# Performance work log

Measured on AMD Instinct MI355X. Metric: run time of the kernel, lower is better.

The kernel has to match this reference:

```python
import jax, jax.numpy as jnp
import numpy as np

N_NODES = 100000
N_EDGES = 800000
N_PAIRS = 500000
IN_DIM = 128
HID_DIM = 128
OUT_DIM = 64


def setup_inputs() -> dict:
    key = jax.random.key(0)
    k = jax.random.split(key, 7)
    x = jax.random.normal(k[0], (N_NODES, IN_DIM), dtype=jnp.float32)
    edge_rows = jax.random.randint(k[1], (N_EDGES,), 0, N_NODES, dtype=jnp.int32)
    edge_cols = jax.random.randint(k[2], (N_EDGES,), 0, N_NODES, dtype=jnp.int32)
    edge_vals = jax.random.uniform(k[3], (N_EDGES,), dtype=jnp.float32)
    pairs = jax.random.randint(k[4], (N_PAIRS, 2), 0, N_NODES, dtype=jnp.int32)
    # Learned params: nn.Linear(in, out, bias=False) -> weight applied as x @ W.T; we store W already transposed.
    W1 = jax.random.normal(k[5], (IN_DIM, HID_DIM), dtype=jnp.float32) / np.sqrt(IN_DIM)
    W2 = jax.random.normal(k[6], (HID_DIM, OUT_DIM), dtype=jnp.float32) / np.sqrt(HID_DIM)
    return {"x": x, "edge_rows": edge_rows, "edge_cols": edge_cols,
            "edge_vals": edge_vals, "pairs": pairs, "W1": W1, "W2": W2}


def reference(x, edge_rows, edge_cols, edge_vals, pairs, W1, W2):
    n = x.shape[0]

    def gcn(h, W):
        # SpMM: out[i] = sum_{e: rows[e]==i} vals[e] * h[cols[e]], then dense linear.
        msgs = edge_vals[:, None] * h[edge_cols]          # [E, d] gather
        agg = jax.ops.segment_sum(msgs, edge_rows, num_segments=n)  # [N, d] scatter
        return agg @ W

    h = jax.nn.relu(gcn(x, W1))
    h = gcn(h, W2)
    # decode: dot product between endpoint embeddings
    return jnp.sum(h[pairs[:, 0]] * h[pairs[:, 1]], axis=-1)  # [P]
```

## Files before the change

### kernel.cpp

```cpp
#include <hip/hip_runtime.h>

#define N_NODES 100000
#define N_EDGES 800000
#define N_PAIRS 500000

#define T_TILE  2048
#define N_TILES ((N_EDGES + T_TILE - 1) / T_TILE)
#define N_BKT   256
#define NPB     391
#define BCAP    4096

typedef _Float16 half4v __attribute__((ext_vector_type(4)));
typedef _Float16 half8v __attribute__((ext_vector_type(8)));
typedef float    f32x4  __attribute__((ext_vector_type(4)));

__device__ __forceinline__ int swz(int byte_off, int row) {
    return byte_off ^ ((row & 7) << 4);
}

template<int M, bool A_IS_F32>
__global__ __launch_bounds__(256) void gemm_mfma(const void* __restrict__ Ap,
                                                 const _Float16* __restrict__ Wt,
                                                 _Float16* __restrict__ C, int nRows) {
    constexpr int K  = 128;
    constexpr int CT = M / 16;
    __shared__ _Float16 Alds[64 * K];
    __shared__ _Float16 Wlds[M * K];

    const int rb = blockIdx.x * 64;

    if (A_IS_F32) {
        const float* A = (const float*)Ap;
        for (int idx = threadIdx.x; idx < 64 * (K / 4); idx += 256) {
            const int row = idx >> 5, c4 = idx & 31;
            const int rg = (rb + row < nRows) ? rb + row : nRows - 1;
            const float4 a = *(const float4*)&A[(long)rg * K + c4 * 4];
            half4v h = { (_Float16)a.x, (_Float16)a.y, (_Float16)a.z, (_Float16)a.w };
            *(half4v*)((char*)Alds + swz(row * 256 + c4 * 8, row)) = h;
        }
    } else {
        const _Float16* A = (const _Float16*)Ap;
        for (int idx = threadIdx.x; idx < 64 * (K / 8); idx += 256) {
            const int row = idx >> 4, seg = idx & 15;
            const int rg = (rb + row < nRows) ? rb + row : nRows - 1;
            const half8v h = *(const half8v*)&A[(long)rg * K + seg * 8];
            *(half8v*)((char*)Alds + swz(row * 256 + seg * 16, row)) = h;
        }
    }
    for (int idx = threadIdx.x; idx < M * (K / 8); idx += 256) {
        const int col = idx >> 4, seg = idx & 15;
        const half8v h = *(const half8v*)&Wt[col * K + seg * 8];
        *(half8v*)((char*)Wlds + swz(col * 256 + seg * 16, col)) = h;
    }
    __syncthreads();

    const int l  = threadIdx.x & 63;
    const int w  = threadIdx.x >> 6;
    const int lr = l & 15;
    const int lg = l >> 4;

    f32x4 acc[CT];
    #pragma unroll
    for (int ct = 0; ct < CT; ++ct) acc[ct] = (f32x4){0.f, 0.f, 0.f, 0.f};

    #pragma unroll
    for (int ks = 0; ks < K / 16; ++ks) {
        const int kb   = ks * 32 + lg * 8;
        const int arow = w * 16 + lr;
        const half4v af = *(const half4v*)((const char*)Alds + swz(arow * 256 + kb, arow));
        #pragma unroll
        for (int ct = 0; ct < CT; ++ct) {
            const int col = ct * 16 + lr;
            const half4v bf = *(const half4v*)((const char*)Wlds + swz(col * 256 + kb, col));
            acc[ct] = __builtin_amdgcn_mfma_f32_16x16x16f16(af, bf, acc[ct], 0, 0, 0);
        }
    }

    #pragma unroll
    for (int ct = 0; ct < CT; ++ct) {
        const int col = ct * 16 + lr;
        #pragma unroll
        for (int j = 0; j < 4; ++j) {
            const int row = rb + w * 16 + lg * 4 + j;
            if (row < nRows) C[(long)row * M + col] = (_Float16)acc[ct][j];
        }
    }
}

__global__ __launch_bounds__(512) void spmm_gemm_fused(const int* __restrict__ rowptr,
                                                       const long long* __restrict__ epack,
                                                       const _Float16* __restrict__ g,
                                                       const _Float16* __restrict__ Wt2,
                                                       _Float16* __restrict__ g2, int nRows) {
    constexpr int K = 128, M = 64;
    __shared__ _Float16 Alds[64 * K];
    __shared__ _Float16 Wlds[M * K];

    const int rb = blockIdx.x * 64;

    for (int idx = threadIdx.x; idx < M * (K / 8); idx += 512) {
        const int col = idx >> 4, seg = idx & 15;
        const half8v h = *(const half8v*)&Wt2[col * K + seg * 8];
        *(half8v*)((char*)Wlds + swz(col * 256 + seg * 16, col)) = h;
    }

    const int li = threadIdx.x & 15;
    const int rs = threadIdx.x >> 4;
    #pragma unroll
    for (int s = 0; s < 2; ++s) {
        const int lrow = s * 32 + rs;
        const int r  = rb + lrow;
        const int rc = (r < nRows) ? r : nRows - 1;
        const int lo = rowptr[rc], hi = rowptr[rc + 1];
        float acc[8] = {0.f, 0.f, 0.f, 0.f, 0.f, 0.f, 0.f, 0.f};
        #pragma unroll 4
        for (int e = lo; e < hi; ++e) {
            const long long pk = epack[e];
            const int   c = (int)pk;
            const float v = __int_as_float((int)(pk >> 32));
            const half8v m = *(const half8v*)&g[(long)c * K + li * 8];
            #pragma unroll
            for (int j = 0; j < 8; ++j) acc[j] += v * (float)m[j];
        }
        half8v h;
        #pragma unroll
        for (int j = 0; j < 8; ++j) h[j] = (_Float16)fmaxf(acc[j], 0.f);
        *(half8v*)((char*)Alds + swz(lrow * 256 + li * 16, lrow)) = h;
    }
    __syncthreads();

    const int l    = threadIdx.x & 63;
    const int w    = threadIdx.x >> 6;
    const int lr   = l & 15;
    const int lg   = l >> 4;
    const int rowg = w >> 1;
    const int colb = (w & 1) * 32;

    f32x4 acc[2];
    acc[0] = (f32x4){0.f, 0.f, 0.f, 0.f};
    acc[1] = (f32x4){0.f, 0.f, 0.f, 0.f};

    #pragma unroll
    for (int ks = 0; ks < K / 16; ++ks) {
        const int kb   = ks * 32 + lg * 8;
        const int arow = rowg * 16 + lr;
        const half4v af = *(const half4v*)((const char*)Alds + swz(arow * 256 + kb, arow));
        #pragma unroll
        for (int ct = 0; ct < 2; ++ct) {
            const int col = colb + ct * 16 + lr;
            const half4v bf = *(const half4v*)((const char*)Wlds + swz(col * 256 + kb, col));
            acc[ct] = __builtin_amdgcn_mfma_f32_16x16x16f16(af, bf, acc[ct], 0, 0, 0);
        }
    }

    #pragma unroll
    for (int ct = 0; ct < 2; ++ct) {
        const int col = colb + ct * 16 + lr;
        #pragma unroll
        for (int j = 0; j < 4; ++j) {
            const int row = rb + rowg * 16 + lg * 4 + j;
            if (row < nRows) g2[(long)row * M + col] = (_Float16)acc[ct][j];
        }
    }
}

__global__ __launch_bounds__(256) void hist_both(const int* __restrict__ erows,
                                                 int* __restrict__ hist,
                                                 const float* __restrict__ W1,
                                                 const float* __restrict__ W2,
                                                 _Float16* __restrict__ Wt1,
                                                 _Float16* __restrict__ Wt2) {
    if (blockIdx.x == N_TILES) {
        for (int i = threadIdx.x; i < 128 * 128; i += 256) {
            const int k = i >> 7, m = i & 127;
            Wt1[m * 128 + k] = (_Float16)W1[i];
        }
        for (int i = threadIdx.x; i < 128 * 64; i += 256) {
            const int k = i >> 6, m = i & 63;
            Wt2[m * 128 + k] = (_Float16)W2[i];
        }
        return;
    }
    __shared__ int cnt[N_BKT];
    cnt[threadIdx.x] = 0;
    __syncthreads();
    const int e0 = blockIdx.x * T_TILE;
    const int e1 = min(e0 + T_TILE, N_EDGES);
    for (int e = e0 + threadIdx.x; e < e1; e += 256)
        atomicAdd(&cnt[erows[e] / NPB], 1);
    __syncthreads();
    hist[blockIdx.x * N_BKT + threadIdx.x] = cnt[threadIdx.x];
}

__global__ __launch_bounds__(512) void bucket_scan(const int* __restrict__ hist,
                                                   int* __restrict__ offpart,
                                                   int* __restrict__ bt) {
    __shared__ int lds[512];
    const int b = blockIdx.x;
    const int t = threadIdx.x;
    const int v = (t < N_TILES) ? hist[t * N_BKT + b] : 0;
    lds[t] = v;
    __syncthreads();
    for (int o = 1; o < 512; o <<= 1) {
        int u = (t >= o) ? lds[t - o] : 0;
        __syncthreads();
        lds[t] += u;
        __syncthreads();
    }
    if (t < N_TILES) offpart[b * N_TILES + t] = lds[t] - v;
    if (t == 511) bt[b] = lds[511];
}

__global__ __launch_bounds__(256) void bkt_base(const int* __restrict__ bt,
                                                int* __restrict__ bbase) {
    __shared__ int lds[256];
    const int t = threadIdx.x;
    const int v = bt[t];
    lds[t] = v;
    __syncthreads();
    for (int o = 1; o < 256; o <<= 1) {
        int u = (t >= o) ? lds[t - o] : 0;
        __syncthreads();
        lds[t] += u;
        __syncthreads();
    }
    bbase[t] = lds[t] - v;
    if (t == 255) bbase[256] = lds[255];
}

__global__ __launch_bounds__(256) void partition(const int* __restrict__ erows,
                                                 const int* __restrict__ ecols,
                                                 const float* __restrict__ evals,
                                                 const int* __restrict__ offpart,
                                                 const int* __restrict__ bbase,
                                                 unsigned long long* __restrict__ etmp) {
    __shared__ int cur[N_BKT];
    cur[threadIdx.x] = bbase[threadIdx.x] + offpart[threadIdx.x * N_TILES + blockIdx.x];
    __syncthreads();
    const int e0 = blockIdx.x * T_TILE;
    const int e1 = min(e0 + T_TILE, N_EDGES);
    for (int e = e0 + threadIdx.x; e < e1; e += 256) {
        const int r = erows[e];
        const int b = r / NPB;
        const int lrow = r - b * NPB;
        const int p = atomicAdd(&cur[b], 1);
        etmp[p] = ((unsigned long long)(unsigned)__float_as_int(evals[e]) << 32)
                | ((unsigned)lrow << 17) | (unsigned)ecols[e];
    }
}

__global__ __launch_bounds__(256) void bucket_reorder(const int* __restrict__ bbase,
                                                      const unsigned long long* __restrict__ etmp,
                                                      unsigned long long* __restrict__ epack,
                                                      int* __restrict__ rowptr) {
    __shared__ int lcnt[NPB + 1];
    __shared__ int psum[256];
    __shared__ int lcur[NPB];
    __shared__ unsigned long long stg[BCAP];
    const int b    = blockIdx.x;
    const int t    = threadIdx.x;
    const int lo   = b * NPB;
    const int hiN  = min(lo + NPB, N_NODES);
    const int nloc = hiN - lo;
    const int base = bbase[b];
    const int cnt  = bbase[b + 1] - base;

    for (int j = t; j < NPB; j += 256) lcnt[j] = 0;
    __syncthreads();
    for (int i = t; i < cnt; i += 256)
        atomicAdd(&lcnt[(int)((etmp[base + i] >> 17) & 0x1FF)], 1);
    __syncthreads();
    const int j0 = 2 * t, j1 = 2 * t + 1;
    const int a0 = (j0 < NPB) ? lcnt[j0] : 0;
    const int a1 = (j1 < NPB) ? lcnt[j1] : 0;
    psum[t] = a0 + a1;
    __syncthreads();
    for (int o = 1; o < 256; o <<= 1) {
        int u = (t >= o) ? psum[t - o] : 0;
        __syncthreads();
        psum[t] += u;
        __syncthreads();
    }
    const int ex0 = psum[t] - (a0 + a1);
    const int ex1 = ex0 + a0;
    if (j0 < NPB) lcur[j0] = ex0;
    if (j1 < NPB) lcur[j1] = ex1;
    if (j0 < nloc) rowptr[lo + j0] = base + ex0;
    if (j1 < nloc) rowptr[lo + j1] = base + ex1;
    if (b == N_BKT - 1 && t == 0) rowptr[N_NODES] = N_EDGES;
    __syncthreads();
    for (int i = t; i < cnt; i += 256) {
        const unsigned long long p = etmp[base + i];
        const int lrow = (int)((p >> 17) & 0x1FF);
        const int pos  = atomicAdd(&lcur[lrow], 1);
        const unsigned long long rec = (p & 0xFFFFFFFF00000000ULL) | (p & 0x1FFFFULL);
        if (pos < BCAP) stg[pos] = rec;
        else epack[base + pos] = rec;
    }
    __syncthreads();
    const int n = min(cnt, BCAP);
    for (int i = t; i < n; i += 256)
        epack[base + i] = stg[i];
}

template<int D, bool RELU>
__global__ __launch_bounds__(256) void spmm_csr_h(const int* __restrict__ rowptr,
                                                  const long long* __restrict__ epack,
                                                  const _Float16* __restrict__ g,
                                                  _Float16* __restrict__ agg, int nRows) {
    constexpr int LPR = D / 8;
    constexpr int RPB = 256 / LPR;
    const int r  = blockIdx.x * RPB + threadIdx.x / LPR;
    const int li = threadIdx.x % LPR;
    if (r >= nRows) return;
    const int lo = rowptr[r], hi = rowptr[r + 1];
    float acc[8] = {0.f, 0.f, 0.f, 0.f, 0.f, 0.f, 0.f, 0.f};
    #pragma unroll 4
    for (int e = lo; e < hi; ++e) {
        const long long pk = epack[e];
        const int   c = (int)pk;
        const float v = __int_as_float((int)(pk >> 32));
        const half8v m = *(const half8v*)&g[(long)c * D + li * 8];
        #pragma unroll
        for (int j = 0; j < 8; ++j) acc[j] += v * (float)m[j];
    }
    half8v o;
    #pragma unroll
    for (int j = 0; j < 8; ++j) {
        float a = RELU ? fmaxf(acc[j], 0.f) : acc[j];
        o[j] = (_Float16)a;
    }
    *(half8v*)&agg[(long)r * D + li * 8] = o;
}

__global__ __launch_bounds__(256) void decode_dot(const _Float16* __restrict__ h2,
                                                  const int2* __restrict__ pairs,
                                                  float* __restrict__ out, int nPairs) {
    const int tid  = blockIdx.x * 256 + threadIdx.x;
    const int half = (nPairs + 1) / 2;
    const int p0   = tid >> 3;
    const int lane = tid & 7;
    if (p0 >= half) return;
    const int p1 = p0 + half;
    const bool has1 = p1 < nPairs;
    const int2 pr0 = pairs[p0];
    const int2 pr1 = has1 ? pairs[p1] : pr0;
    const half8v a0 = *(const half8v*)&h2[(long)pr0.x * 64 + lane * 8];
    const half8v b0 = *(const half8v*)&h2[(long)pr0.y * 64 + lane * 8];
    const half8v a1 = *(const half8v*)&h2[(long)pr1.x * 64 + lane * 8];
    const half8v b1 = *(const half8v*)&h2[(long)pr1.y * 64 + lane * 8];
    float s0 = 0.f, s1 = 0.f;
    #pragma unroll
    for (int j = 0; j < 8; ++j) {
        s0 += (float)a0[j] * (float)b0[j];
        s1 += (float)a1[j] * (float)b1[j];
    }
    s0 += __shfl_xor(s0, 1); s1 += __shfl_xor(s1, 1);
    s0 += __shfl_xor(s0, 2); s1 += __shfl_xor(s1, 2);
    s0 += __shfl_xor(s0, 4); s1 += __shfl_xor(s1, 4);
    if (lane == 0) {
        out[p0] = s0;
        if (has1) out[p1] = s1;
    }
}

extern "C" void kernel_launch(void* const* d_in, const int* in_sizes, int n_in,
                              void* d_out, int out_size, void* d_ws, size_t ws_size,
                              hipStream_t stream) {
    const float* x     = (const float*)d_in[0];
    const int*   erows = (const int*)d_in[1];
    const int*   ecols = (const int*)d_in[2];
    const float* evals = (const float*)d_in[3];
    const int2*  pairs = (const int2*)d_in[4];
    const float* W1    = (const float*)d_in[5];
    const float* W2    = (const float*)d_in[6];
    float* out = (float*)d_out;

    char* ws = (char*)d_ws;
    _Float16*           g1      = (_Float16*)          (ws);
    _Float16*           g2      = (_Float16*)          (ws + 25600000);
    _Float16*           agg2    = (_Float16*)          (ws + 38400000);
    int*                rowptr  = (int*)               (ws + 51200000);
    unsigned long long* epack   = (unsigned long long*)(ws + 51600016);
    _Float16*           Wt1     = (_Float16*)          (ws + 58000016);
    _Float16*           Wt2     = (_Float16*)          (ws + 58032784);
    int*                hist    = (int*)               (ws + 58049168);
    int*                offpart = (int*)               (ws + 58449552);
    int*                bt      = (int*)               (ws + 58849936);
    int*                bbase   = (int*)               (ws + 58850960);
    unsigned long long* etmp    = (unsigned long long*)(ws + 58852016);

    hist_both<<<N_TILES + 1, 256, 0, stream>>>(erows, hist, W1, W2, Wt1, Wt2);
    bucket_scan<<<N_BKT, 512, 0, stream>>>(hist, offpart, bt);
    bkt_base<<<1, 256, 0, stream>>>(bt, bbase);
    partition<<<N_TILES, 256, 0, stream>>>(erows, ecols, evals, offpart, bbase, etmp);
    bucket_reorder<<<N_BKT, 256, 0, stream>>>(bbase, etmp, epack, rowptr);

    gemm_mfma<128, true><<<(N_NODES + 63) / 64, 256, 0, stream>>>(x, Wt1, g1, N_NODES);

    spmm_gemm_fused<<<(N_NODES + 63) / 64, 512, 0, stream>>>(
        rowptr, (const long long*)epack, g1, Wt2, g2, N_NODES);

    spmm_csr_h<64, false><<<(N_NODES + 31) / 32, 256, 0, stream>>>(
        rowptr, (const long long*)epack, g2, agg2, N_NODES);

    decode_dot<<<((N_PAIRS + 1) / 2 * 8 + 255) / 256, 256, 0, stream>>>(
        agg2, pairs, out, N_PAIRS);
}
```

Before: 146.0 us.

## Merge bucket reorder with first GEMM and fold bucket base scan into scan

Puts the bucket_reorder work and the first dense GEMM into one launch, with the block index picking which role a block plays. The bkt_base kernel is removed: the last block of bucket_scan, found through an atomic done counter with threadfences, computes the bucket bases. This cuts two kernel launches and lets the independent reorder and GEMM work share the GPU. In exchange, every block reserves 48KB of shared memory, which may lower GEMM occupancy, and the last-block pattern adds an atomic and fences.

```diff
diff --git a/kernel.cpp b/kernel.cpp
--- a/kernel.cpp
+++ b/kernel.cpp
@@ -9,6 +9,7 @@
 #define N_BKT   256
 #define NPB     391
 #define BCAP    4096
+#define GEMM_BLKS ((N_NODES + 63) / 64)
 
 typedef _Float16 half4v __attribute__((ext_vector_type(4)));
 typedef _Float16 half8v __attribute__((ext_vector_type(8)));
@@ -18,44 +19,91 @@
     return byte_off ^ ((row & 7) << 4);
 }
 
-template<int M, bool A_IS_F32>
-__global__ __launch_bounds__(256) void gemm_mfma(const void* __restrict__ Ap,
-                                                 const _Float16* __restrict__ Wt,
-                                                 _Float16* __restrict__ C, int nRows) {
-    constexpr int K  = 128;
-    constexpr int CT = M / 16;
-    __shared__ _Float16 Alds[64 * K];
-    __shared__ _Float16 Wlds[M * K];
-
-    const int rb = blockIdx.x * 64;
-
-    if (A_IS_F32) {
-        const float* A = (const float*)Ap;
-        for (int idx = threadIdx.x; idx < 64 * (K / 4); idx += 256) {
-            const int row = idx >> 5, c4 = idx & 31;
-            const int rg = (rb + row < nRows) ? rb + row : nRows - 1;
-            const float4 a = *(const float4*)&A[(long)rg * K + c4 * 4];
-            half4v h = { (_Float16)a.x, (_Float16)a.y, (_Float16)a.z, (_Float16)a.w };
-            *(half4v*)((char*)Alds + swz(row * 256 + c4 * 8, row)) = h;
-        }
-    } else {
-        const _Float16* A = (const _Float16*)Ap;
-        for (int idx = threadIdx.x; idx < 64 * (K / 8); idx += 256) {
-            const int row = idx >> 4, seg = idx & 15;
-            const int rg = (rb + row < nRows) ? rb + row : nRows - 1;
-            const half8v h = *(const half8v*)&A[(long)rg * K + seg * 8];
-            *(half8v*)((char*)Alds + swz(row * 256 + seg * 16, row)) = h;
-        }
-    }
-    for (int idx = threadIdx.x; idx < M * (K / 8); idx += 256) {
+__global__ __launch_bounds__(256) void reorder_and_gemm(
+        const int* __restrict__ bbase,
+        const unsigned long long* __restrict__ etmp,
+        unsigned long long* __restrict__ epack,
+        int* __restrict__ rowptr,
+        const float* __restrict__ x,
+        const _Float16* __restrict__ Wt1,
+        _Float16* __restrict__ g1, int nRows) {
+    __shared__ __align__(16) char smem[49152];
+    const int t = threadIdx.x;
+
+    if (blockIdx.x < N_BKT) {
+        int*                lcnt = (int*)smem;
+        int*                psum = (int*)(smem + 1600);
+        int*                lcur = (int*)(smem + 2624);
+        unsigned long long* stg  = (unsigned long long*)(smem + 4224);
+
+        const int b    = blockIdx.x;
+        const int lo   = b * NPB;
+        const int hiN  = min(lo + NPB, N_NODES);
+        const int nloc = hiN - lo;
+        const int base = bbase[b];
+        const int cnt  = bbase[b + 1] - base;
+
+        for (int j = t; j < NPB; j += 256) lcnt[j] = 0;
+        __syncthreads();
+        for (int i = t; i < cnt; i += 256)
+            atomicAdd(&lcnt[(int)((etmp[base + i] >> 17) & 0x1FF)], 1);
+        __syncthreads();
+        const int j0 = 2 * t, j1 = 2 * t + 1;
+        const int a0 = (j0 < NPB) ? lcnt[j0] : 0;
+        const int a1 = (j1 < NPB) ? lcnt[j1] : 0;
+        psum[t] = a0 + a1;
+        __syncthreads();
+        for (int o = 1; o < 256; o <<= 1) {
+            int u = (t >= o) ? psum[t - o] : 0;
+            __syncthreads();
+            psum[t] += u;
+            __syncthreads();
+        }
+        const int ex0 = psum[t] - (a0 + a1);
+        const int ex1 = ex0 + a0;
+        if (j0 < NPB) lcur[j0] = ex0;
+        if (j1 < NPB) lcur[j1] = ex1;
+        if (j0 < nloc) rowptr[lo + j0] = base + ex0;
+        if (j1 < nloc) rowptr[lo + j1] = base + ex1;
+        if (b == N_BKT - 1 && t == 0) rowptr[N_NODES] = N_EDGES;
+        __syncthreads();
+        for (int i = t; i < cnt; i += 256) {
+            const unsigned long long p = etmp[base + i];
+            const int lrow = (int)((p >> 17) & 0x1FF);
+            const int pos  = atomicAdd(&lcur[lrow], 1);
+            const unsigned long long rec = (p & 0xFFFFFFFF00000000ULL) | (p & 0x1FFFFULL);
+            if (pos < BCAP) stg[pos] = rec;
+            else epack[base + pos] = rec;
+        }
+        __syncthreads();
+        const int n = min(cnt, BCAP);
+        for (int i = t; i < n; i += 256)
+            epack[base + i] = stg[i];
+        return;
+    }
+
+    constexpr int K = 128, M = 128, CT = M / 16;
+    _Float16* Alds = (_Float16*)smem;
+    _Float16* Wlds = (_Float16*)(smem + 16384);
+
+    const int rb = (blockIdx.x - N_BKT) * 64;
+
+    for (int idx = t; idx < 64 * (K / 4); idx += 256) {
+        const int row = idx >> 5, c4 = idx & 31;
+        const int rg = (rb + row < nRows) ? rb + row : nRows - 1;
+        const float4 a = *(const float4*)&x[(long)rg * K + c4 * 4];
+        half4v h = { (_Float16)a.x, (_Float16)a.y, (_Float16)a.z, (_Float16)a.w };
+        *(half4v*)((char*)Alds + swz(row * 256 + c4 * 8, row)) = h;
+    }
+    for (int idx = t; idx < M * (K / 8); idx += 256) {
         const int col = idx >> 4, seg = idx & 15;
-        const half8v h = *(const half8v*)&Wt[col * K + seg * 8];
+        const half8v h = *(const half8v*)&Wt1[col * K + seg * 8];
         *(half8v*)((char*)Wlds + swz(col * 256 + seg * 16, col)) = h;
     }
     __syncthreads();
 
-    const int l  = threadIdx.x & 63;
-    const int w  = threadIdx.x >> 6;
+    const int l  = t & 63;
+    const int w  = t >> 6;
     const int lr = l & 15;
     const int lg = l >> 4;
 
@@ -82,7 +130,7 @@
         #pragma unroll
         for (int j = 0; j < 4; ++j) {
             const int row = rb + w * 16 + lg * 4 + j;
-            if (row < nRows) C[(long)row * M + col] = (_Float16)acc[ct][j];
+            if (row < nRows) g1[(long)row * M + col] = (_Float16)acc[ct][j];
         }
     }
 }
@@ -169,8 +217,10 @@
                                                  const float* __restrict__ W1,
                                                  const float* __restrict__ W2,
                                                  _Float16* __restrict__ Wt1,
-                                                 _Float16* __restrict__ Wt2) {
+                                                 _Float16* __restrict__ Wt2,
+                                                 int* __restrict__ done) {
     if (blockIdx.x == N_TILES) {
+        if (threadIdx.x == 0) *done = 0;
         for (int i = threadIdx.x; i < 128 * 128; i += 256) {
             const int k = i >> 7, m = i & 127;
             Wt1[m * 128 + k] = (_Float16)W1[i];
@@ -194,7 +244,9 @@
 
 __global__ __launch_bounds__(512) void bucket_scan(const int* __restrict__ hist,
                                                    int* __restrict__ offpart,
-                                                   int* __restrict__ bt) {
+                                                   int* __restrict__ bt,
+                                                   int* __restrict__ bbase,
+                                                   int* __restrict__ done) {
     __shared__ int lds[512];
     const int b = blockIdx.x;
     const int t = threadIdx.x;
@@ -209,23 +261,29 @@
     }
     if (t < N_TILES) offpart[b * N_TILES + t] = lds[t] - v;
     if (t == 511) bt[b] = lds[511];
-}
-
-__global__ __launch_bounds__(256) void bkt_base(const int* __restrict__ bt,
-                                                int* __restrict__ bbase) {
-    __shared__ int lds[256];
-    const int t = threadIdx.x;
-    const int v = bt[t];
-    lds[t] = v;
-    __syncthreads();
-    for (int o = 1; o < 256; o <<= 1) {
-        int u = (t >= o) ? lds[t - o] : 0;
-        __syncthreads();
-        lds[t] += u;
-        __syncthreads();
-    }
-    bbase[t] = lds[t] - v;
-    if (t == 255) bbase[256] = lds[255];
+
+    __shared__ int lastf;
+    __syncthreads();
+    if (t == 0) {
+        __threadfence();
+        lastf = (atomicAdd(done, 1) == gridDim.x - 1) ? 1 : 0;
+    }
+    __syncthreads();
+    if (lastf) {
+        __threadfence();
+        __shared__ int lds2[256];
+        int bv = 0;
+        if (t < 256) { bv = bt[t]; lds2[t] = bv; }
+        __syncthreads();
+        for (int o = 1; o < 256; o <<= 1) {
+            int u = (t < 256 && t >= o) ? lds2[t - o] : 0;
+            __syncthreads();
+            if (t < 256) lds2[t] += u;
+            __syncthreads();
+        }
+        if (t < 256) bbase[t] = lds2[t] - bv;
+        if (t == 255) bbase[256] = lds2[255];
+    }
 }
 
 __global__ __launch_bounds__(256) void partition(const int* __restrict__ erows,
@@ -247,60 +305,6 @@
         etmp[p] = ((unsigned long long)(unsigned)__float_as_int(evals[e]) << 32)
                 | ((unsigned)lrow << 17) | (unsigned)ecols[e];
     }
-}
-
-__global__ __launch_bounds__(256) void bucket_reorder(const int* __restrict__ bbase,
-                                                      const unsigned long long* __restrict__ etmp,
-                                                      unsigned long long* __restrict__ epack,
-                                                      int* __restrict__ rowptr) {
-    __shared__ int lcnt[NPB + 1];
-    __shared__ int psum[256];
-    __shared__ int lcur[NPB];
-    __shared__ unsigned long long stg[BCAP];
-    const int b    = blockIdx.x;
-    const int t    = threadIdx.x;
-    const int lo   = b * NPB;
-    const int hiN  = min(lo + NPB, N_NODES);
-    const int nloc = hiN - lo;
-    const int base = bbase[b];
-    const int cnt  = bbase[b + 1] - base;
-
-    for (int j = t; j < NPB; j += 256) lcnt[j] = 0;
-    __syncthreads();
-    for (int i = t; i < cnt; i += 256)
-        atomicAdd(&lcnt[(int)((etmp[base + i] >> 17) & 0x1FF)], 1);
-    __syncthreads();
-    const int j0 = 2 * t, j1 = 2 * t + 1;
-    const int a0 = (j0 < NPB) ? lcnt[j0] : 0;
-    const int a1 = (j1 < NPB) ? lcnt[j1] : 0;
-    psum[t] = a0 + a1;
-    __syncthreads();
-    for (int o = 1; o < 256; o <<= 1) {
-        int u = (t >= o) ? psum[t - o] : 0;
-        __syncthreads();
-        psum[t] += u;
-        __syncthreads();
-    }
-    const int ex0 = psum[t] - (a0 + a1);
-    const int ex1 = ex0 + a0;
-    if (j0 < NPB) lcur[j0] = ex0;
-    if (j1 < NPB) lcur[j1] = ex1;
-    if (j0 < nloc) rowptr[lo + j0] = base + ex0;
-    if (j1 < nloc) rowptr[lo + j1] = base + ex1;
-    if (b == N_BKT - 1 && t == 0) rowptr[N_NODES] = N_EDGES;
-    __syncthreads();
-    for (int i = t; i < cnt; i += 256) {
-        const unsigned long long p = etmp[base + i];
-        const int lrow = (int)((p >> 17) & 0x1FF);
-        const int pos  = atomicAdd(&lcur[lrow], 1);
-        const unsigned long long rec = (p & 0xFFFFFFFF00000000ULL) | (p & 0x1FFFFULL);
-        if (pos < BCAP) stg[pos] = rec;
-        else epack[base + pos] = rec;
-    }
-    __syncthreads();
-    const int n = min(cnt, BCAP);
-    for (int i = t; i < n; i += 256)
-        epack[base + i] = stg[i];
 }
 
 template<int D, bool RELU>
@@ -388,17 +392,17 @@
     int*                offpart = (int*)               (ws + 58449552);
     int*                bt      = (int*)               (ws + 58849936);
     int*                bbase   = (int*)               (ws + 58850960);
-    unsigned long long* etmp    = (unsigned long long*)(ws + 58852016);
-
-    hist_both<<<N_TILES + 1, 256, 0, stream>>>(erows, hist, W1, W2, Wt1, Wt2);
-    bucket_scan<<<N_BKT, 512, 0, stream>>>(hist, offpart, bt);
-    bkt_base<<<1, 256, 0, stream>>>(bt, bbase);
+    int*                done    = (int*)               (ws + 58852016);
+    unsigned long long* etmp    = (unsigned long long*)(ws + 58852032);
+
+    hist_both<<<N_TILES + 1, 256, 0, stream>>>(erows, hist, W1, W2, Wt1, Wt2, done);
+    bucket_scan<<<N_BKT, 512, 0, stream>>>(hist, offpart, bt, bbase, done);
     partition<<<N_TILES, 256, 0, stream>>>(erows, ecols, evals, offpart, bbase, etmp);
-    bucket_reorder<<<N_BKT, 256, 0, stream>>>(bbase, etmp, epack, rowptr);
-
-    gemm_mfma<128, true><<<(N_NODES + 63) / 64, 256, 0, stream>>>(x, Wt1, g1, N_NODES);
-
-    spmm_gemm_fused<<<(N_NODES + 63) / 64, 512, 0, stream>>>(
+
+    reorder_and_gemm<<<N_BKT + GEMM_BLKS, 256, 0, stream>>>(
+        bbase, etmp, epack, rowptr, x, Wt1, g1, N_NODES);
+
+    spmm_gemm_fused<<<GEMM_BLKS, 512, 0, stream>>>(
         rowptr, (const long long*)epack, g1, Wt2, g2, N_NODES);
 
     spmm_csr_h<64, false><<<(N_NODES + 31) / 32, 256, 0, stream>>>(
```

Result: faster. 140.6 us (-3.7%).
